# Kernel tuning notes

Measured on AMD Instinct MI355X. Metric: run time of the kernel, lower is better.

The kernel has to match this reference:

```python
import jax, jax.numpy as jnp
import numpy as np
from jax import lax

V, F, B = 25000, 8192, 1024  # vertices, faces, block size (batch_size)
EPS = 1e-8

def setup_inputs() -> dict:
    key = jax.random.key(0)
    k1, k2, k3 = jax.random.split(key, 3)
    vertices = jax.random.normal(k1, (V, 3), dtype=jnp.float32)
    faces = jax.random.randint(k2, (F, 3), 0, V, dtype=jnp.int64)
    face_probs = jax.random.uniform(k3, (F,), dtype=jnp.float32)
    return {"vertices": vertices, "faces": faces, "face_probs": face_probs}

def reference(vertices, faces, face_probs):
    nF = faces.shape[0]
    # edges = cat([ (f0,f1), (f1,f2), (f2,f0) ])  -> [E,2], E = 3F
    edges = jnp.concatenate([faces[:, [0, 1]], faces[:, [1, 2]], faces[:, [2, 0]]], axis=0)
    # Faithful to source: edge_to_face = arange(F).repeat_interleave(3)
    edge_to_face = jnp.repeat(jnp.arange(nF), 3)
    edge_points = vertices[edges]              # [E,2,3]
    centroids = edge_points.mean(axis=1)       # [E,3]
    E = edges.shape[0]
    v_all = edge_points[:, 1] - edge_points[:, 0] + EPS  # edge directions + eps, [E,3]
    starts = edge_points[:, 0]                 # [E,3] (unused by count but kept for clarity)
    col_idx = jnp.arange(E)

    def block(carry, b):
        row_cnt, col_cnt = carry
        i0 = b * B
        c_blk = lax.dynamic_slice(centroids, (i0, 0), (B, 3))   # [B,3]
        v1 = lax.dynamic_slice(v_all, (i0, 0), (B, 3))          # [B,3]
        # pairwise L2 distances [B,E]
        d2 = ((c_blk[:, None, :] - centroids[None, :, :]) ** 2).sum(-1)
        dists = jnp.sqrt(d2)
        pair = (dists < 1.0 + 1e-6) & ((i0 + jnp.arange(B))[:, None] < col_idx[None, :])
        # cross2 = cross(v1, v2); crossing iff ||cross2||+eps > 1e-5
        cross2 = jnp.cross(v1[:, None, :], v_all[None, :, :])   # [B,E,3]
        norm2 = jnp.sqrt((cross2 ** 2).sum(-1)) + EPS
        # after clamp t in [0,1] always, so crossings = pair & valid
        crossings = (pair & (norm2 > 1e-5)).astype(jnp.float32)
        row_cnt = lax.dynamic_update_slice(row_cnt, crossings.sum(1), (i0,))
        col_cnt = col_cnt + crossings.sum(0)
        return (row_cnt, col_cnt), None

    init = (jnp.zeros(E, jnp.float32), jnp.zeros(E, jnp.float32))
    (row_cnt, col_cnt), _ = lax.scan(block, init, jnp.arange(E // B))
    cnt_per_edge = row_cnt + col_cnt           # times edge appears as e1 or e2 in a crossing
    crossing_count = jax.ops.segment_sum(cnt_per_edge, edge_to_face, num_segments=nF)
    crossing_count = jnp.clip(crossing_count, 0.0, 100.0)
    return (face_probs * crossing_count).mean()
```

## Files before the change

kernel.cpp:

```cpp
#include <hip/hip_runtime.h>

#define V_ 25000
#define F_ 8192
#define E_ (3 * F_)

constexpr int CAP  = 101;
constexpr int GD   = 8;
constexpr int NC   = GD*GD*GD;
constexpr int CAPC = 6144;
constexpr int FLATCAP = 384;

constexpr int CR_BLOCKS = 256;
constexpr int CR_TPB    = 1024;
constexpr int CR_WPB    = CR_TPB / 64;
constexpr int CR_NW     = CR_BLOCKS * CR_WPB;

constexpr size_t OFF_LIST  = 393216;
constexpr size_t OFF_CCNT  = 50724864;
constexpr size_t OFF_NDONE = OFF_CCNT + 2048;
constexpr size_t OFF_CNT   = OFF_CCNT + 4096;

__device__ const int PPAT[26][3] = {
    { 1, 1, 1},
    { 1, 1, 0},{ 1, 0, 1},{ 0, 1, 1},
    { 1, 0, 0},{ 0, 1, 0},{ 0, 0, 1},{ 1, 1,-1},{ 1,-1, 1},{-1, 1, 1},
    { 1,-1, 0},{ 1, 0,-1},{ 0, 1,-1},{-1, 1, 0},{-1, 0, 1},{ 0,-1, 1},
    {-1, 0, 0},{ 0,-1, 0},{ 0, 0,-1},{-1,-1, 1},{-1, 1,-1},{ 1,-1,-1},
    {-1,-1, 0},{-1, 0,-1},{ 0,-1,-1},
    {-1,-1,-1}
};

__device__ __forceinline__ int cell_coord(float c)
{
    return min(GD-1, max(0, (int)floorf(c) + GD/2));
}

__global__ __launch_bounds__(256) void build_kernel(
    const float* __restrict__ vertices, const int* __restrict__ faces,
    float4* __restrict__ C4, float4* __restrict__ cellList,
    int* __restrict__ cellCount)
{
    __shared__ int lh[NC];
    __shared__ int lbase[NC];
    for (int i = threadIdx.x; i < NC; i += 256) lh[i] = 0;
    __syncthreads();

    const int e = blockIdx.x * 256 + threadIdx.x;
    int f, i0, i1;
    if (e < F_)        { f = e;        i0 = 0; i1 = 1; }
    else if (e < 2*F_) { f = e - F_;   i0 = 1; i1 = 2; }
    else               { f = e - 2*F_; i0 = 2; i1 = 0; }
    int a = faces[f*3 + i0];
    int b = faces[f*3 + i1];
    float cx = 0.5f*(vertices[a*3+0] + vertices[b*3+0]);
    float cy = 0.5f*(vertices[a*3+1] + vertices[b*3+1]);
    float cz = 0.5f*(vertices[a*3+2] + vertices[b*3+2]);
    int cell = (cell_coord(cz)*GD + cell_coord(cy))*GD + cell_coord(cx);
    int rank = atomicAdd(&lh[cell], 1);
    __syncthreads();
    for (int i = threadIdx.x; i < NC; i += 256) {
        int c = lh[i];
        if (c) lbase[i] = atomicAdd(&cellCount[i], c);
    }
    __syncthreads();
    C4[e] = make_float4(cx, cy, cz, __int_as_float(cell));
    cellList[(size_t)cell * CAPC + lbase[cell] + rank] = make_float4(cx, cy, cz, 0.f);
}

__device__ __forceinline__ int count_edge(
    int e, const float4* __restrict__ C4, const float4* __restrict__ cellList,
    const int* __restrict__ cellCount, unsigned* flat, int lane)
{
    float4 s = C4[e];
    const float ex = s.x, ey = s.y, ez = s.z;
    const int   cell = __float_as_int(s.w);
    const int ix = cell & 7, iy = (cell >> 3) & 7, iz = cell >> 6;
    const float d2t = (1.0f + 1e-6f) * (1.0f + 1e-6f);

    int count = 0;

    {
        const int n = cellCount[cell];
        const float4* __restrict__ L = cellList + (size_t)cell * CAPC;
        float4 cur = L[lane];
        for (int base = 0;;) {
            int nb = base + 64;
            bool more = nb < n;
            float4 nxt;
            if (more) nxt = L[nb + lane];
            float dx = ex - cur.x, dy = ey - cur.y, dz = ez - cur.z;
            float d2 = dx*dx + dy*dy + dz*dz;
            bool c = (base + lane < n) && (d2 < d2t);
            count += __popcll(__ballot(c));
            if (count >= CAP) goto done;
            if (!more) break;
            cur = nxt; base = nb;
        }
    }

    {
        const int dirx = (ix <= 3) ? 1 : -1;
        const int diry = (iy <= 3) ? 1 : -1;
        const int dirz = (iz <= 3) ? 1 : -1;

        int cq = 0, nq = 0, cellq = cell;
        if (lane < 26) {
            int ox = PPAT[lane][0] * dirx;
            int oy = PPAT[lane][1] * diry;
            int oz = PPAT[lane][2] * dirz;
            int x = ix + ox, y = iy + oy, z = iz + oz;
            if (((unsigned)x < (unsigned)GD) & ((unsigned)y < (unsigned)GD) &
                ((unsigned)z < (unsigned)GD)) {
                cellq = cell + oz*64 + oy*8 + ox;
                nq = cellCount[cellq];
                cq = (nq + 63) >> 6;
            }
        }
        int incl = cq;
#pragma unroll
        for (int d = 1; d < 64; d <<= 1) {
            int t = __shfl_up(incl, d, 64);
            if (lane >= d) incl += t;
        }
        const int T = __shfl(incl, 63);
        const int excl = incl - cq;

        if (T == 0) goto done;

        if (T > FLATCAP) {
            for (int q = 0; q < 26; ++q) {
                int ox = PPAT[q][0] * dirx, oy = PPAT[q][1] * diry,
                    oz = PPAT[q][2] * dirz;
                int x = ix + ox, y = iy + oy, z = iz + oz;
                if (((unsigned)x >= (unsigned)GD) | ((unsigned)y >= (unsigned)GD) |
                    ((unsigned)z >= (unsigned)GD)) continue;
                int nc2 = cell + oz*64 + oy*8 + ox;
                int n = cellCount[nc2];
                const float4* __restrict__ L = cellList + (size_t)nc2 * CAPC;
                for (int base = 0; base < n; base += 64) {
                    float4 t4 = L[base + lane];
                    float dx = ex - t4.x, dy = ey - t4.y, dz = ez - t4.z;
                    float d2 = dx*dx + dy*dy + dz*dz;
                    bool c = (base + lane < n) && (d2 < d2t);
                    count += __popcll(__ballot(c));
                    if (count >= CAP) goto done;
                }
            }
            goto done;
        }

        for (int k = 0; k < cq; ++k)
            flat[excl + k] =
                ((unsigned)cellq << 14) | ((unsigned)k << 7)
                | (unsigned)min(64, nq - k*64);
        {
            int pi = T + lane;
            if (pi < T + 12) flat[pi] = (unsigned)cell << 14;
        }
        asm volatile("s_waitcnt lgkmcnt(0)" ::: "memory");

        const int Tp = (T + 3) & ~3;

#define FADDR(E) (cellList + (size_t)((E) >> 14) * CAPC + (((E) >> 7) & 127) * 64 + lane)
#define PROC(B, EN)                                                        \
        {                                                                  \
            float dx = ex - (B).x, dy = ey - (B).y, dz = ez - (B).z;       \
            float d2 = dx*dx + dy*dy + dz*dz;                              \
            bool c = (lane < (int)((EN) & 127u)) && (d2 < d2t);            \
            count += __popcll(__ballot(c));                                \
            if (count >= CAP) goto done;                                   \
        }

        unsigned e0 = flat[0], e1 = flat[1], e2 = flat[2], e3 = flat[3];
        float4 b0 = *FADDR(e0), b1 = *FADDR(e1), b2 = *FADDR(e2), b3 = *FADDR(e3);
        for (int j = 0;; j += 4) {
            unsigned f0 = flat[j+4], f1 = flat[j+5], f2 = flat[j+6], f3 = flat[j+7];
            float4 n0 = *FADDR(f0), n1 = *FADDR(f1),
                   n2 = *FADDR(f2), n3 = *FADDR(f3);
            PROC(b0, e0) PROC(b1, e1) PROC(b2, e2) PROC(b3, e3)
            if (j + 4 >= Tp) break;
            e0 = f0; e1 = f1; e2 = f2; e3 = f3;
            b0 = n0; b1 = n1; b2 = n2; b3 = n3;
        }
#undef FADDR
#undef PROC
    }
done:
    return count;
}

__global__ __launch_bounds__(1024) void count_reduce_kernel(
    const float4* __restrict__ C4, const float4* __restrict__ cellList,
    const int* __restrict__ cellCount, int* __restrict__ cnt,
    const float* __restrict__ probs, int* __restrict__ ndone,
    float* __restrict__ out)
{
    __shared__ unsigned flatLDS[CR_WPB][FLATCAP + 16];
    __shared__ float wsum[CR_WPB];
    __shared__ int lastFlag;
    const int wave = threadIdx.x >> 6;
    const int lane = threadIdx.x & 63;

    for (int e = blockIdx.x * CR_WPB + wave; e < E_; e += CR_NW) {
        int c = count_edge(e, C4, cellList, cellCount, flatLDS[wave], lane);
        if (lane == 0) cnt[e] = c;
    }
    __syncthreads();
    if (threadIdx.x == 0) {
        __threadfence();
        int old = __hip_atomic_fetch_add(ndone, 1, __ATOMIC_ACQ_REL,
                                         __HIP_MEMORY_SCOPE_AGENT);
        lastFlag = (old == CR_BLOCKS - 1);
    }
    __syncthreads();
    if (!lastFlag) return;

    __threadfence();
    float local = 0.0f;
    for (int f = threadIdx.x; f < F_; f += CR_TPB) {
        int c0 = __hip_atomic_load(&cnt[f],        __ATOMIC_RELAXED, __HIP_MEMORY_SCOPE_AGENT);
        int c1 = __hip_atomic_load(&cnt[F_ + f],   __ATOMIC_RELAXED, __HIP_MEMORY_SCOPE_AGENT);
        int c2 = __hip_atomic_load(&cnt[2*F_ + f], __ATOMIC_RELAXED, __HIP_MEMORY_SCOPE_AGENT);
        float c = (float)(c0 + c1 + c2);
        c = fminf(fmaxf(c, 0.0f), 100.0f);
        local += probs[f] * c;
    }
#pragma unroll
    for (int off = 32; off > 0; off >>= 1)
        local += __shfl_down(local, off, 64);
    if (lane == 0) wsum[wave] = local;
    __syncthreads();
    if (threadIdx.x == 0) {
        float t = 0.0f;
#pragma unroll
        for (int w = 0; w < CR_WPB; w++) t += wsum[w];
        out[0] = t / (float)F_;
    }
}

extern "C" void kernel_launch(void* const* d_in, const int* in_sizes, int n_in,
                              void* d_out, int out_size, void* d_ws, size_t ws_size,
                              hipStream_t stream)
{
    const float* vertices = (const float*)d_in[0];
    const int*   faces    = (const int*)d_in[1];
    const float* probs    = (const float*)d_in[2];
    float* out = (float*)d_out;

    char* ws = (char*)d_ws;
    float4* C4        = (float4*)ws;
    float4* cellList  = (float4*)(ws + OFF_LIST);
    int*    cellCount = (int*)(ws + OFF_CCNT);
    int*    ndone     = (int*)(ws + OFF_NDONE);
    int*    cnt       = (int*)(ws + OFF_CNT);

    hipMemsetAsync(cellCount, 0, 4096, stream);
    hipLaunchKernelGGL(build_kernel, dim3(E_ / 256), dim3(256), 0, stream,
                       vertices, faces, C4, cellList, cellCount);
    hipLaunchKernelGGL(count_reduce_kernel, dim3(CR_BLOCKS), dim3(CR_TPB), 0, stream,
                       C4, cellList, cellCount, cnt, probs, ndone, out);
}
```

Baseline: 105.1 us.

## Launch one wave per edge with hierarchical completion counters for final reduction

Replaces the grid-stride persistent kernel (256 blocks of 1024 threads) with 6144 small blocks of 256 threads, each handling four edges, one per wave. The aim is to balance load dynamically across edges whose neighbour-cell work varies. To avoid 6144 blocks contending on one atomic counter, completion is tracked with 64 padded group counters and a second-level counter that selects the last block to do the final reduction. The cost is more block launches and two atomics in some blocks.

```diff
diff --git a/kernel.cpp b/kernel.cpp
--- a/kernel.cpp
+++ b/kernel.cpp
@@ -10,15 +10,16 @@
 constexpr int CAPC = 6144;
 constexpr int FLATCAP = 384;
 
-constexpr int CR_BLOCKS = 256;
-constexpr int CR_TPB    = 1024;
-constexpr int CR_WPB    = CR_TPB / 64;
-constexpr int CR_NW     = CR_BLOCKS * CR_WPB;
-
-constexpr size_t OFF_LIST  = 393216;
-constexpr size_t OFF_CCNT  = 50724864;
-constexpr size_t OFF_NDONE = OFF_CCNT + 2048;
-constexpr size_t OFF_CNT   = OFF_CCNT + 4096;
+constexpr int CNT_BLOCKS = E_ / 4;
+constexpr int GROUPS     = 64;
+constexpr int PER_GROUP  = CNT_BLOCKS / GROUPS;
+
+constexpr size_t OFF_LIST = 393216;
+constexpr size_t OFF_CCNT = 50724864;
+constexpr size_t OFF_ND1  = OFF_CCNT + 2048;
+constexpr size_t OFF_ND2  = OFF_ND1 + 8192;
+constexpr size_t OFF_CNT  = OFF_ND2 + 128;
+constexpr size_t ZERO_BYTES = 2048 + 8192 + 128;
 
 __device__ const int PPAT[26][3] = {
     { 1, 1, 1},
@@ -189,53 +190,56 @@
     return count;
 }
 
-__global__ __launch_bounds__(1024) void count_reduce_kernel(
+__global__ __launch_bounds__(256) void count_kernel(
     const float4* __restrict__ C4, const float4* __restrict__ cellList,
     const int* __restrict__ cellCount, int* __restrict__ cnt,
-    const float* __restrict__ probs, int* __restrict__ ndone,
-    float* __restrict__ out)
-{
-    __shared__ unsigned flatLDS[CR_WPB][FLATCAP + 16];
-    __shared__ float wsum[CR_WPB];
+    const float* __restrict__ probs, int* __restrict__ ndone1,
+    int* __restrict__ ndone2, float* __restrict__ out)
+{
+    __shared__ unsigned flatLDS[4][FLATCAP + 16];
+    __shared__ float wsum[4];
     __shared__ int lastFlag;
     const int wave = threadIdx.x >> 6;
     const int lane = threadIdx.x & 63;
-
-    for (int e = blockIdx.x * CR_WPB + wave; e < E_; e += CR_NW) {
-        int c = count_edge(e, C4, cellList, cellCount, flatLDS[wave], lane);
-        if (lane == 0) cnt[e] = c;
-    }
+    const int e = blockIdx.x * 4 + wave;
+
+    int c = count_edge(e, C4, cellList, cellCount, flatLDS[wave], lane);
+    if (lane == 0) cnt[e] = c;
+
     __syncthreads();
     if (threadIdx.x == 0) {
         __threadfence();
-        int old = __hip_atomic_fetch_add(ndone, 1, __ATOMIC_ACQ_REL,
-                                         __HIP_MEMORY_SCOPE_AGENT);
-        lastFlag = (old == CR_BLOCKS - 1);
+        int g = blockIdx.x & (GROUPS - 1);
+        int lf = 0;
+        int o1 = __hip_atomic_fetch_add(&ndone1[g * 32], 1, __ATOMIC_ACQ_REL,
+                                        __HIP_MEMORY_SCOPE_AGENT);
+        if (o1 == PER_GROUP - 1) {
+            int o2 = __hip_atomic_fetch_add(ndone2, 1, __ATOMIC_ACQ_REL,
+                                            __HIP_MEMORY_SCOPE_AGENT);
+            lf = (o2 == GROUPS - 1);
+        }
+        lastFlag = lf;
     }
     __syncthreads();
     if (!lastFlag) return;
 
     __threadfence();
     float local = 0.0f;
-    for (int f = threadIdx.x; f < F_; f += CR_TPB) {
+    for (int f = threadIdx.x; f < F_; f += 256) {
         int c0 = __hip_atomic_load(&cnt[f],        __ATOMIC_RELAXED, __HIP_MEMORY_SCOPE_AGENT);
         int c1 = __hip_atomic_load(&cnt[F_ + f],   __ATOMIC_RELAXED, __HIP_MEMORY_SCOPE_AGENT);
         int c2 = __hip_atomic_load(&cnt[2*F_ + f], __ATOMIC_RELAXED, __HIP_MEMORY_SCOPE_AGENT);
-        float c = (float)(c0 + c1 + c2);
-        c = fminf(fmaxf(c, 0.0f), 100.0f);
-        local += probs[f] * c;
+        float fc = (float)(c0 + c1 + c2);
+        fc = fminf(fmaxf(fc, 0.0f), 100.0f);
+        local += probs[f] * fc;
     }
 #pragma unroll
     for (int off = 32; off > 0; off >>= 1)
         local += __shfl_down(local, off, 64);
     if (lane == 0) wsum[wave] = local;
     __syncthreads();
-    if (threadIdx.x == 0) {
-        float t = 0.0f;
-#pragma unroll
-        for (int w = 0; w < CR_WPB; w++) t += wsum[w];
-        out[0] = t / (float)F_;
-    }
+    if (threadIdx.x == 0)
+        out[0] = (wsum[0] + wsum[1] + wsum[2] + wsum[3]) / (float)F_;
 }
 
 extern "C" void kernel_launch(void* const* d_in, const int* in_sizes, int n_in,
@@ -251,12 +255,13 @@
     float4* C4        = (float4*)ws;
     float4* cellList  = (float4*)(ws + OFF_LIST);
     int*    cellCount = (int*)(ws + OFF_CCNT);
-    int*    ndone     = (int*)(ws + OFF_NDONE);
+    int*    ndone1    = (int*)(ws + OFF_ND1);
+    int*    ndone2    = (int*)(ws + OFF_ND2);
     int*    cnt       = (int*)(ws + OFF_CNT);
 
-    hipMemsetAsync(cellCount, 0, 4096, stream);
+    hipMemsetAsync(cellCount, 0, ZERO_BYTES, stream);
     hipLaunchKernelGGL(build_kernel, dim3(E_ / 256), dim3(256), 0, stream,
                        vertices, faces, C4, cellList, cellCount);
-    hipLaunchKernelGGL(count_reduce_kernel, dim3(CR_BLOCKS), dim3(CR_TPB), 0, stream,
-                       C4, cellList, cellCount, cnt, probs, ndone, out);
-}
+    hipLaunchKernelGGL(count_kernel, dim3(CNT_BLOCKS), dim3(256), 0, stream,
+                       C4, cellList, cellCount, cnt, probs, ndone1, ndone2, out);
+}
```

After: 286.9 us. 2.73x slower.
